# Performance work log

Measured on AMD Instinct MI355X. Metric: run time of the kernel, lower is better.

Reference implementation:

```python
import jax, jax.numpy as jnp
import numpy as np

E = 8          # num_experts
K = 2          # top_k
CAP = 0.8      # capacity_ratio
LN_EPS = 1e-6


def setup_inputs() -> dict:
    key = jax.random.key(0)
    ks = jax.random.split(key, 6)
    N, C, H, W = 64, 384, 32, 32
    Hd = 4 * C
    x = jax.random.normal(ks[0], (N, C, H, W), jnp.float32)
    conv_w = jax.random.normal(ks[1], (7, 7, 1, C), jnp.float32) * 0.05  # HWIO, depthwise
    conv_b = jnp.zeros((C,), jnp.float32)
    ln_g = jnp.ones((C,), jnp.float32)
    ln_b = jnp.zeros((C,), jnp.float32)
    gate_w = jax.random.normal(ks[2], (E, C), jnp.float32) * 0.02
    w1 = jax.random.normal(ks[3], (E, C, Hd), jnp.float32) * 0.02
    b1 = jnp.zeros((E, Hd), jnp.float32)
    w2 = jax.random.normal(ks[4], (E, Hd, C), jnp.float32) * 0.02
    b2 = jnp.zeros((E, C), jnp.float32)
    layer_scale = jnp.ones((C, 1, 1), jnp.float32) * 1e-6
    return dict(x=x, conv_w=conv_w, conv_b=conv_b, ln_g=ln_g, ln_b=ln_b,
                gate_w=gate_w, w1=w1, b1=b1, w2=w2, b2=b2, layer_scale=layer_scale)


def reference(x, conv_w, conv_b, ln_g, ln_b, gate_w, w1, b1, w2, b2, layer_scale):
    N, C, H, W = x.shape
    # depthwise 7x7 conv, pad 3
    h = jax.lax.conv_general_dilated(
        x, conv_w, window_strides=(1, 1), padding=[(3, 3), (3, 3)],
        dimension_numbers=('NCHW', 'HWIO', 'NCHW'), feature_group_count=C)
    h = h + conv_b[None, :, None, None]
    h = h.transpose(0, 2, 3, 1)  # NHWC
    # LayerNorm over channels
    mu = h.mean(-1, keepdims=True)
    var = ((h - mu) ** 2).mean(-1, keepdims=True)
    h = (h - mu) * jax.lax.rsqrt(var + LN_EPS) * ln_g + ln_b

    T = N * H * W
    x_flat = h.reshape(T, C)

    # Router (eval mode: no aux loss)
    logits = x_flat @ gate_w.T                    # [T, E]
    probs = jax.nn.softmax(logits, axis=-1)
    priority = probs.max(-1)                       # [T]
    topv, topi = jax.lax.top_k(logits, K)          # [T, K]
    weights = jax.nn.softmax(topv, axis=-1)        # [T, K]
    order = jnp.argsort(-priority)                 # descending priority

    # Dispatch: layout k-major like torch (order.repeat(K), topi[order].T.reshape(-1))
    token_idx = jnp.tile(order, K)                 # [M]
    expert_id = topi[order].T.reshape(-1)          # [M]
    gate = weights[order].T.reshape(-1)            # [M]
    M = K * T
    perm = jnp.argsort(expert_id, stable=True)
    token_idx = token_idx[perm]
    expert_id = expert_id[perm]
    gate = gate[perm]

    Be = int(round(K * T * CAP / E))               # static capacity per expert
    counts = jnp.bincount(expert_id, length=E)
    starts = jnp.cumsum(counts) - counts
    pos = jnp.arange(M) - starts[expert_id]
    keep = pos < Be
    slot = jnp.where(keep, expert_id * Be + pos, E * Be)  # dropped -> trash slot

    disp_tok = jnp.zeros((E * Be + 1,), jnp.int32).at[slot].set(token_idx.astype(jnp.int32))
    disp_gate = jnp.zeros((E * Be + 1,), x_flat.dtype).at[slot].set(gate)
    disp_tok = disp_tok[:-1].reshape(E, Be)
    disp_gate = disp_gate[:-1].reshape(E, Be)      # 0 for unfilled slots

    # Grouped expert MLP
    x_e = x_flat[disp_tok]                         # [E, Be, C]
    hid = jax.nn.gelu(jnp.einsum('ebc,ech->ebh', x_e, w1) + b1[:, None, :], approximate=False)
    y = (jnp.einsum('ebh,ehc->ebc', hid, w2) + b2[:, None, :]) * disp_gate[:, :, None]

    # Combine (scatter-add); unfilled slots contribute 0 (gate==0)
    out = jnp.zeros((T, C), x_flat.dtype).at[disp_tok.reshape(-1)].add(y.reshape(-1, C))

    out = out.reshape(N, H, W, C).transpose(0, 3, 1, 2)  # back to NCHW
    return x + layer_scale[None] * out
```

## Files before the change

kernel.cpp:

```cpp
#include <hip/hip_runtime.h>


typedef unsigned int u32;
typedef unsigned long long u64;
typedef unsigned short u16;
typedef __attribute__((ext_vector_type(8))) __bf16 bf16x8;
typedef __attribute__((ext_vector_type(4))) float f32x4;

#define T_TOK 65536
#define C_DIM 384
#define HD 1536
#define BE 13107
#define BP 13184

__device__ __forceinline__ u16 f2bf(float f) {
  u32 u = __float_as_uint(f);
  u32 r = (u + 0x7FFFu + ((u >> 16) & 1u)) >> 16;
  return (u16)r;
}
__device__ __forceinline__ float bf2f(u16 b) { return __uint_as_float(((u32)b) << 16); }

__device__ __forceinline__ u32 cvtpk(float a, float b) {
  u32 r;
  asm("v_cvt_pk_bf16_f32 %0, %1, %2" : "=v"(r) : "v"(a), "v"(b));
  return r;
}

__device__ __forceinline__ void gl16(const void* g, void* l) {
  __builtin_amdgcn_global_load_lds((const __attribute__((address_space(1))) void*)g,
                                   (__attribute__((address_space(3))) void*)l, 16, 0, 0);
}

__global__ __launch_bounds__(256) void k_conv(const float* __restrict__ x,
                                              const float* __restrict__ cw,
                                              const float* __restrict__ cb,
                                              float* __restrict__ hconv) {
  __shared__ float xp[38 * 38];
  int b = blockIdx.x;
  int c = b % 384;
  int tid = threadIdx.x;
  float w49[49];
#pragma unroll
  for (int i = 0; i < 49; i++) w49[i] = cw[i * 384 + c];
  float bias = cb[c];
  for (int i = tid; i < 38 * 38; i += 256) xp[i] = 0.0f;
  __syncthreads();
  const float* xsrc = x + (size_t)b * 1024;
  {
    float4 v = *(const float4*)&xsrc[tid * 4];
    int yy = tid >> 3, xx = (tid & 7) * 4;
    float* d = &xp[(yy + 3) * 38 + xx + 3];
    d[0] = v.x; d[1] = v.y; d[2] = v.z; d[3] = v.w;
  }
  __syncthreads();
  int cl = tid & 31, r0 = (tid >> 5) << 2;
  float o0 = bias, o1 = bias, o2 = bias, o3 = bias;
  const float* colbase = &xp[r0 * 38 + cl];
#pragma unroll
  for (int kx = 0; kx < 7; kx++) {
    float v[10];
#pragma unroll
    for (int k = 0; k < 10; k++) v[k] = colbase[k * 38 + kx];
#pragma unroll
    for (int ky = 0; ky < 7; ky++) {
      float wt = w49[ky * 7 + kx];
      o0 += wt * v[ky + 0];
      o1 += wt * v[ky + 1];
      o2 += wt * v[ky + 2];
      o3 += wt * v[ky + 3];
    }
  }
  float* dst = &hconv[(size_t)b * 1024 + r0 * 32 + cl];
  dst[0] = o0;
  dst[32] = o1;
  dst[64] = o2;
  dst[96] = o3;
}

__global__ __launch_bounds__(256) void k_ln(const float* __restrict__ hconv,
                                            const float* __restrict__ lng,
                                            const float* __restrict__ lnb,
                                            u16* __restrict__ xln) {
  __shared__ float tile[384 * 33];
  int nb = blockIdx.x;
  int n = nb >> 5, y = nb & 31;
  int tid = threadIdx.x;
  const float* src = hconv + (size_t)n * 384 * 1024 + (y << 5);
  for (int i = tid; i < 12288; i += 256) {
    int c = i >> 5, w = i & 31;
    tile[c * 33 + w] = src[(size_t)c * 1024 + w];
  }
  __syncthreads();
  int wv = tid >> 6, lane = tid & 63;
  for (int w = wv; w < 32; w += 4) {
    float v[6];
    float s = 0.f, s2 = 0.f;
#pragma unroll
    for (int k = 0; k < 6; k++) {
      float t = tile[(lane + (k << 6)) * 33 + w];
      v[k] = t; s += t; s2 += t * t;
    }
#pragma unroll
    for (int off = 32; off > 0; off >>= 1) {
      s += __shfl_xor(s, off, 64);
      s2 += __shfl_xor(s2, off, 64);
    }
    float mu = s * (1.0f / 384.0f);
    float var = s2 * (1.0f / 384.0f) - mu * mu;
    float r = rsqrtf(var + 1e-6f);
    size_t t0 = ((size_t)nb << 5) + w;
#pragma unroll
    for (int k = 0; k < 6; k++) {
      int c = lane + (k << 6);
      float o = (v[k] - mu) * r * lng[c] + lnb[c];
      xln[t0 * 384 + c] = f2bf(o);
    }
  }
}

__global__ __launch_bounds__(256) void k_router(const u16* __restrict__ xln,
                                                const float* __restrict__ gw,
                                                u32* __restrict__ keys, u32* __restrict__ vals,
                                                u32* __restrict__ topi,
                                                float* __restrict__ g1, float* __restrict__ g2) {
  __shared__ float gwl[8 * 384];
  int tid = threadIdx.x;
  for (int i = tid; i < 3072; i += 256) gwl[i] = gw[i];
  __syncthreads();
  int wv = tid >> 6, lane = tid & 63;
  int t = (blockIdx.x << 2) + wv;
  float acc[8] = {0, 0, 0, 0, 0, 0, 0, 0};
#pragma unroll
  for (int k = 0; k < 6; k++) {
    int c = lane + (k << 6);
    float xv = bf2f(xln[(size_t)t * 384 + c]);
#pragma unroll
    for (int e = 0; e < 8; e++) acc[e] += xv * gwl[e * 384 + c];
  }
#pragma unroll
  for (int off = 32; off > 0; off >>= 1) {
#pragma unroll
    for (int e = 0; e < 8; e++) acc[e] += __shfl_xor(acc[e], off, 64);
  }
  if (lane == 0) {
    float v1 = -1e30f, v2 = -1e30f;
    int e1 = 0, e2 = 0;
#pragma unroll
    for (int e = 0; e < 8; e++) {
      float l = acc[e];
      if (l > v1) { v2 = v1; e2 = e1; v1 = l; e1 = e; }
      else if (l > v2) { v2 = l; e2 = e; }
    }
    float sum = 0.f;
#pragma unroll
    for (int e = 0; e < 8; e++) sum += __expf(acc[e] - v1);
    float p = 1.0f / sum;
    float ew = __expf(v2 - v1);
    float w1 = 1.0f / (1.0f + ew);
    keys[t] = (~__float_as_uint(p)) >> 16;
    vals[t] = (u32)t;
    topi[t] = (u32)e1 | ((u32)e2 << 8);
    g1[t] = w1;
    g2[t] = ew * w1;
  }
}

__global__ __launch_bounds__(256) void k_hist(const u32* __restrict__ keys,
                                              u32* __restrict__ hist, int shift) {
  __shared__ u32 h[256];
  int tid = threadIdx.x;
  h[tid] = 0;
  __syncthreads();
  u32 key = keys[((size_t)blockIdx.x << 8) + tid];
  atomicAdd(&h[(key >> shift) & 255u], 1u);
  __syncthreads();
  hist[(size_t)tid * gridDim.x + blockIdx.x] = h[tid];
}

__global__ __launch_bounds__(256) void k_scan_rows(u32* __restrict__ data,
                                                   u32* __restrict__ totals, int nb) {
  __shared__ u32 ws[256];
  int d = blockIdx.x, tid = threadIdx.x;
  int seg = nb >> 8;
  u32 base = (u32)d * nb + tid * seg;
  u32 v[2] = {0, 0};
  u32 s = 0;
  for (int i = 0; i < seg; i++) { v[i] = data[base + i]; s += v[i]; }
  ws[tid] = s;
  __syncthreads();
  for (int dd = 1; dd < 256; dd <<= 1) {
    u32 t = (tid >= dd) ? ws[tid - dd] : 0u;
    __syncthreads();
    ws[tid] += t;
    __syncthreads();
  }
  if (tid == 255) totals[d] = ws[255];
  u32 run = (tid > 0) ? ws[tid - 1] : 0u;
  for (int i = 0; i < seg; i++) {
    u32 tmp = v[i];
    data[base + i] = run;
    run += tmp;
  }
}

__global__ __launch_bounds__(256) void k_scan_digits(const u32* __restrict__ totals,
                                                     u32* __restrict__ dbase) {
  __shared__ u32 ws[256];
  int tid = threadIdx.x;
  ws[tid] = totals[tid];
  __syncthreads();
  for (int dd = 1; dd < 256; dd <<= 1) {
    u32 t = (tid >= dd) ? ws[tid - dd] : 0u;
    __syncthreads();
    ws[tid] += t;
    __syncthreads();
  }
  dbase[tid] = (tid > 0) ? ws[tid - 1] : 0u;
}

__global__ __launch_bounds__(256) void k_scatter(const u32* __restrict__ kin,
                                                 const u32* __restrict__ vin,
                                                 u32* __restrict__ kout, u32* __restrict__ vout,
                                                 const u32* __restrict__ scanned,
                                                 const u32* __restrict__ dbase, int shift) {
  __shared__ u32 cnt[4 * 256];
  int tid = threadIdx.x;
  int w = tid >> 6, l = tid & 63;
  int g = (blockIdx.x << 8) + tid;
  u32 key = kin[g], val = vin[g];
  u32 d = (key >> shift) & 255u;
  for (int i = tid; i < 1024; i += 256) cnt[i] = 0u;
  __syncthreads();
  u64 match = ~0ull;
#pragma unroll
  for (int b = 0; b < 8; b++) {
    int bit = (d >> b) & 1;
    u64 bal = __ballot(bit);
    match &= bit ? bal : ~bal;
  }
  u32 rw = __popcll(match & ((1ull << l) - 1ull));
  if (rw == 0) cnt[(w << 8) + d] = (u32)__popcll(match);
  __syncthreads();
  u32 pre = 0;
  for (int w2 = 0; w2 < w; w2++) pre += cnt[(w2 << 8) + d];
  u32 pos = dbase[d] + scanned[(size_t)d * gridDim.x + blockIdx.x] + pre + rw;
  kout[pos] = key;
  vout[pos] = val;
}

__global__ __launch_bounds__(256) void k_entries(const u32* __restrict__ order,
                                                 const u32* __restrict__ topi,
                                                 const float* __restrict__ g1,
                                                 const float* __restrict__ g2,
                                                 u32* __restrict__ ee, u32* __restrict__ et,
                                                 float* __restrict__ eg) {
  int m = (blockIdx.x << 8) + threadIdx.x;
  int i = m & 65535, k = m >> 16;
  u32 tok = order[i];
  u32 pk = topi[tok];
  ee[m] = k ? ((pk >> 8) & 255u) : (pk & 255u);
  et[m] = tok;
  eg[m] = k ? g2[tok] : g1[tok];
}

__global__ __launch_bounds__(256) void k_dispatch(const u32* __restrict__ ee,
                                                  const u32* __restrict__ et,
                                                  const float* __restrict__ eg,
                                                  const u32* __restrict__ scanned,
                                                  int* __restrict__ dtok, float* __restrict__ dgate,
                                                  int* __restrict__ inv) {
  __shared__ u32 cnt[4 * 8];
  int tid = threadIdx.x;
  int w = tid >> 6, l = tid & 63;
  int m = (blockIdx.x << 8) + tid;
  u32 e = ee[m];
  if (tid < 32) cnt[tid] = 0u;
  __syncthreads();
  u64 match = ~0ull;
#pragma unroll
  for (int b = 0; b < 3; b++) {
    int bit = (e >> b) & 1;
    u64 bal = __ballot(bit);
    match &= bit ? bal : ~bal;
  }
  u32 rw = __popcll(match & ((1ull << l) - 1ull));
  if (rw == 0) cnt[(w << 3) + e] = (u32)__popcll(match);
  __syncthreads();
  u32 pre = 0;
  for (int w2 = 0; w2 < w; w2++) pre += cnt[(w2 << 3) + e];
  u32 pos = scanned[(size_t)e * gridDim.x + blockIdx.x] + pre + rw;
  if (pos < (u32)BE) {
    int slot = (int)e * BP + (int)pos;
    dtok[slot] = (int)et[m];
    dgate[slot] = eg[m];
    inv[et[m] * 2 + (m >> 16)] = slot;
  }
}

__global__ __launch_bounds__(256) void k_pack(const float* __restrict__ w,
                                              u16* __restrict__ wp, int NKK, int S) {
  __shared__ float tile[32 * 132];
  int e = blockIdx.y;
  int bx = blockIdx.x;
  int by = bx / NKK, kk = bx - by * NKK;
  int tid = threadIdx.x;
  const float* src = w + ((size_t)e * NKK * 32 + (size_t)kk * 32) * S + by * 128;
  for (int i = tid; i < 4096; i += 256) {
    int r = i >> 7, c = i & 127;
    tile[r * 132 + c] = src[(size_t)r * S + c];
  }
  __syncthreads();
  u16* dst = wp + ((size_t)e * gridDim.x + bx) * 4096;
#pragma unroll
  for (int h = 0; h < 2; h++) {
    int f = tid + (h << 8);
    int lane6 = f & 63, grp = f >> 6;
    int m15 = lane6 & 15, kq = lane6 >> 4;
    u16 o[8];
#pragma unroll
    for (int j = 0; j < 8; j++) o[j] = f2bf(tile[(kq * 8 + j) * 132 + grp * 16 + m15]);
    *(uint4*)&dst[f * 8] = *(const uint4*)o;
  }
}

__global__ __launch_bounds__(256) void k_gather(const u16* __restrict__ xln,
                                                const int* __restrict__ dtok,
                                                u16* __restrict__ apack, int e0) {
  __shared__ int stok[128];
  int b = blockIdx.x;
  int zloc = b / 103, bx = b - zloc * 103;
  int e = e0 + zloc;
  int tid = threadIdx.x;
  if (tid < 128) stok[tid] = dtok[e * BP + bx * 128 + tid];
  __syncthreads();
  u16* dst = apack + (size_t)b * 12 * 4096;
  int f0 = tid, f1 = tid + 256;
  int g0 = f0 >> 6, l0 = f0 & 63;
  int g1 = f1 >> 6, l1 = f1 & 63;
  int tokA = stok[g0 * 16 + (l0 & 15)];
  int tokB = stok[g1 * 16 + (l1 & 15)];
  const u16* sA = xln + (size_t)tokA * 384 + (l0 >> 4) * 8;
  const u16* sB = xln + (size_t)tokB * 384 + (l1 >> 4) * 8;
  u16* dA = dst + f0 * 8;
  u16* dB = dst + f1 * 8;
#pragma unroll
  for (int kk = 0; kk < 12; kk++) {
    *(uint4*)(dA + kk * 4096) = *(const uint4*)(sA + kk * 32);
    *(uint4*)(dB + kk * 4096) = *(const uint4*)(sB + kk * 32);
  }
}

__global__ __launch_bounds__(256) void k_gemm1(const u16* __restrict__ apack,
                                               const u16* __restrict__ w1p,
                                               const float* __restrict__ b1,
                                               u16* __restrict__ hid, int e0) {
  __shared__ __align__(16) char smem[49152];
  int tid = threadIdx.x;
  int bid = blockIdx.x;
  int lg = (bid & 7) * 618 + (bid >> 3);
  int z = lg / 1236;
  int rr = lg - z * 1236;
  int bx = rr / 12;
  int by = rr - bx * 12;
  int e = e0 + z;
  int wv = tid >> 6, lane = tid & 63;
  int wm = wv & 1, wn = wv >> 1;
  int quad = lane >> 4, c15 = lane & 15;
  const u16* asrc = apack + ((size_t)(z * 103 + bx) * 12) * 4096;
  const u16* bsrc = w1p + ((size_t)(e * 12 + by) * 12) * 4096;
  float4 bias4[4];
#pragma unroll
  for (int j = 0; j < 4; j++)
    bias4[j] = *(const float4*)&b1[e * HD + by * 128 + wn * 64 + j * 16 + quad * 4];
  f32x4 acc[4][4];
#pragma unroll
  for (int i = 0; i < 4; i++)
#pragma unroll
    for (int j = 0; j < 4; j++) acc[i][j] = (f32x4){0.f, 0.f, 0.f, 0.f};

  char* const bb0 = smem;
  char* const bb1 = smem + 16384;
  char* const bb2 = smem + 32768;

  auto issue = [&](int kk, char* buf) {
    short* As = (short*)buf;
    short* Bs = (short*)(buf + 8192);
    const u16* a = asrc + kk * 4096;
    const u16* b = bsrc + kk * 4096;
    gl16(a + tid * 8, &As[tid * 8]);
    gl16(a + (tid + 256) * 8, &As[(tid + 256) * 8]);
    gl16(b + tid * 8, &Bs[tid * 8]);
    gl16(b + (tid + 256) * 8, &Bs[(tid + 256) * 8]);
  };
  auto compute = [&](char* buf) {
    short* As = (short*)buf;
    short* Bs = (short*)(buf + 8192);
    bf16x8 af[4], bfr[4];
#pragma unroll
    for (int i = 0; i < 4; i++) af[i] = *(const bf16x8*)&As[((((wm << 2) + i) << 6) | lane) * 8];
#pragma unroll
    for (int j = 0; j < 4; j++) bfr[j] = *(const bf16x8*)&Bs[((((wn << 2) + j) << 6) | lane) * 8];
    __builtin_amdgcn_s_setprio(1);
#pragma unroll
    for (int i = 0; i < 4; i++)
#pragma unroll
      for (int j = 0; j < 4; j++)
        acc[i][j] = __builtin_amdgcn_mfma_f32_16x16x32_bf16(bfr[j], af[i], acc[i][j], 0, 0, 0);
    __builtin_amdgcn_s_setprio(0);
  };

  asm volatile("s_waitcnt vmcnt(0) lgkmcnt(0)" ::: "memory");
  __builtin_amdgcn_sched_barrier(0);
  issue(0, bb0);
  issue(1, bb1);
#define STEP1(tt, ib, cb)                                \
  issue(tt + 2, ib);                                     \
  asm volatile("s_waitcnt vmcnt(8)" ::: "memory");       \
  __builtin_amdgcn_sched_barrier(0);                     \
  __builtin_amdgcn_s_barrier();                          \
  compute(cb);                                           \
  __builtin_amdgcn_s_barrier();
  for (int t0 = 0; t0 < 9; t0 += 3) {
    STEP1(t0, bb2, bb0)
    STEP1(t0 + 1, bb0, bb1)
    STEP1(t0 + 2, bb1, bb2)
  }
  STEP1(9, bb2, bb0)
#undef STEP1
  asm volatile("s_waitcnt vmcnt(4)" ::: "memory");
  __builtin_amdgcn_sched_barrier(0);
  __builtin_amdgcn_s_barrier();
  compute(bb1);
  asm volatile("s_waitcnt vmcnt(0)" ::: "memory");
  __builtin_amdgcn_sched_barrier(0);
  __builtin_amdgcn_s_barrier();
  compute(bb2);
  __syncthreads();

  u16* prp = (u16*)smem + wv * 4608;
#pragma unroll
  for (int j = 0; j < 4; j++) {
    float4 b4 = bias4[j];
    int ncol = j * 16 + quad * 4;
#pragma unroll
    for (int i = 0; i < 4; i++) {
      int mrow = i * 16 + c15;
      float v0 = acc[i][j][0] + b4.x;
      float v1 = acc[i][j][1] + b4.y;
      float v2 = acc[i][j][2] + b4.z;
      float v3 = acc[i][j][3] + b4.w;
      v0 *= __builtin_amdgcn_rcpf(1.0f + __expf(-1.702f * v0));
      v1 *= __builtin_amdgcn_rcpf(1.0f + __expf(-1.702f * v1));
      v2 *= __builtin_amdgcn_rcpf(1.0f + __expf(-1.702f * v2));
      v3 *= __builtin_amdgcn_rcpf(1.0f + __expf(-1.702f * v3));
      uint2 pk;
      pk.x = cvtpk(v0, v1);
      pk.y = cvtpk(v2, v3);
      *(uint2*)&prp[mrow * 72 + ncol] = pk;
    }
  }
  u16* hb = hid + ((size_t)(z * 103 + bx) * 48 + by * 4 + wn * 2) * 4096 + (wm * 4) * 512 + lane * 8;
#pragma unroll
  for (int k2 = 0; k2 < 2; k2++)
#pragma unroll
    for (int gs = 0; gs < 4; gs++) {
      uint4 v = *(const uint4*)&prp[(gs * 16 + c15) * 72 + k2 * 32 + quad * 8];
      *(uint4*)(hb + (size_t)k2 * 4096 + gs * 512) = v;
    }
}

__global__ __launch_bounds__(256) void k_gemm2(const u16* __restrict__ hid,
                                               const u16* __restrict__ w2p,
                                               const float* __restrict__ b2,
                                               const float* __restrict__ dgate,
                                               u16* __restrict__ yb, int e0) {
  __shared__ __align__(16) char smem[49152];
  int tid = threadIdx.x;
  int bid = blockIdx.x;
  int xcd = bid & 7;
  int lg = xcd * 154 + (xcd < 4 ? xcd : 4) + (bid >> 3);
  int z = lg / 309;
  int rr = lg - z * 309;
  int bx = rr / 3;
  int byn = rr - bx * 3;
  int e = e0 + z;
  int wv = tid >> 6, lane = tid & 63;
  int wm = wv & 1, wn = wv >> 1;
  int quad = lane >> 4, c15 = lane & 15;
  const u16* asrc = hid + ((size_t)(z * 103 + bx) * 48) * 4096;
  const u16* bsrc = w2p + ((size_t)(e * 3 + byn) * 48) * 4096;
  float4 bias4[4];
#pragma unroll
  for (int j = 0; j < 4; j++)
    bias4[j] = *(const float4*)&b2[e * 384 + byn * 128 + wn * 64 + j * 16 + quad * 4];
  float gv[4];
#pragma unroll
  for (int i = 0; i < 4; i++) gv[i] = dgate[e * BP + bx * 128 + wm * 64 + i * 16 + c15];
  f32x4 acc[4][4];
#pragma unroll
  for (int i = 0; i < 4; i++)
#pragma unroll
    for (int j = 0; j < 4; j++) acc[i][j] = (f32x4){0.f, 0.f, 0.f, 0.f};

  char* const bb0 = smem;
  char* const bb1 = smem + 16384;
  char* const bb2 = smem + 32768;

  auto issue = [&](int kk, char* buf) {
    short* As = (short*)buf;
    short* Bs = (short*)(buf + 8192);
    const u16* a = asrc + kk * 4096;
    const u16* b = bsrc + kk * 4096;
    gl16(a + tid * 8, &As[tid * 8]);
    gl16(a + (tid + 256) * 8, &As[(tid + 256) * 8]);
    gl16(b + tid * 8, &Bs[tid * 8]);
    gl16(b + (tid + 256) * 8, &Bs[(tid + 256) * 8]);
  };
  auto compute = [&](char* buf) {
    short* As = (short*)buf;
    short* Bs = (short*)(buf + 8192);
    bf16x8 af[4], bfr[4];
#pragma unroll
    for (int i = 0; i < 4; i++) af[i] = *(const bf16x8*)&As[((((wm << 2) + i) << 6) | lane) * 8];
#pragma unroll
    for (int j = 0; j < 4; j++) bfr[j] = *(const bf16x8*)&Bs[((((wn << 2) + j) << 6) | lane) * 8];
    __builtin_amdgcn_s_setprio(1);
#pragma unroll
    for (int i = 0; i < 4; i++)
#pragma unroll
      for (int j = 0; j < 4; j++)
        acc[i][j] = __builtin_amdgcn_mfma_f32_16x16x32_bf16(bfr[j], af[i], acc[i][j], 0, 0, 0);
    __builtin_amdgcn_s_setprio(0);
  };

  asm volatile("s_waitcnt vmcnt(0) lgkmcnt(0)" ::: "memory");
  __builtin_amdgcn_sched_barrier(0);
  issue(0, bb0);
  issue(1, bb1);
#define STEP2(tt, ib, cb)                                \
  issue(tt + 2, ib);                                     \
  asm volatile("s_waitcnt vmcnt(8)" ::: "memory");       \
  __builtin_amdgcn_sched_barrier(0);                     \
  __builtin_amdgcn_s_barrier();                          \
  compute(cb);                                           \
  __builtin_amdgcn_s_barrier();
  for (int t0 = 0; t0 < 45; t0 += 3) {
    STEP2(t0, bb2, bb0)
    STEP2(t0 + 1, bb0, bb1)
    STEP2(t0 + 2, bb1, bb2)
  }
  STEP2(45, bb2, bb0)
#undef STEP2
  asm volatile("s_waitcnt vmcnt(4)" ::: "memory");
  __builtin_amdgcn_sched_barrier(0);
  __builtin_amdgcn_s_barrier();
  compute(bb1);
  asm volatile("s_waitcnt vmcnt(0)" ::: "memory");
  __builtin_amdgcn_sched_barrier(0);
  __builtin_amdgcn_s_barrier();
  compute(bb2);
  __syncthreads();

  u16* prp = (u16*)smem + wv * 4608;
#pragma unroll
  for (int j = 0; j < 4; j++) {
    float4 b4 = bias4[j];
    int ncol = j * 16 + quad * 4;
#pragma unroll
    for (int i = 0; i < 4; i++) {
      int mrow = i * 16 + c15;
      float g = gv[i];
      float v0 = (acc[i][j][0] + b4.x) * g;
      float v1 = (acc[i][j][1] + b4.y) * g;
      float v2 = (acc[i][j][2] + b4.z) * g;
      float v3 = (acc[i][j][3] + b4.w) * g;
      uint2 pk;
      pk.x = cvtpk(v0, v1);
      pk.y = cvtpk(v2, v3);
      *(uint2*)&prp[mrow * 72 + ncol] = pk;
    }
  }
  u16* ybase = yb + ((size_t)(e * BP + bx * 128 + wm * 64)) * 384 + byn * 128 + wn * 64;
#pragma unroll
  for (int it = 0; it < 8; it++) {
    int r = it * 8 + (lane >> 3);
    int n0 = (lane & 7) * 8;
    uint4 v = *(const uint4*)&prp[r * 72 + n0];
    *(uint4*)(ybase + (size_t)r * 384 + n0) = v;
  }
}

__global__ __launch_bounds__(256) void k_final(const float* __restrict__ x,
                                               const u16* __restrict__ yb,
                                               const int* __restrict__ inv,
                                               const float* __restrict__ ls,
                                               float* __restrict__ out) {
  __shared__ float tile[32 * 385];
  __shared__ int sl[64];
  int nb = blockIdx.x;
  int n = nb >> 5, yy = nb & 31;
  int tid = threadIdx.x;
  int t0 = nb << 5;
  if (tid < 64) sl[tid] = inv[t0 * 2 + tid];
  __syncthreads();
  for (int idx = tid; idx < 1536; idx += 256) {
    int w = idx / 48;
    int cc = (idx - w * 48) << 3;
    float a[8] = {0, 0, 0, 0, 0, 0, 0, 0};
#pragma unroll
    for (int k = 0; k < 2; k++) {
      int s = sl[(w << 1) + k];
      if (s >= 0) {
        uint4 v = *(const uint4*)&yb[(size_t)s * 384 + cc];
        const u16* pv = (const u16*)&v;
#pragma unroll
        for (int j = 0; j < 8; j++) a[j] += bf2f(pv[j]);
      }
    }
    float* tp = &tile[w * 385 + cc];
#pragma unroll
    for (int j = 0; j < 8; j++) tp[j] = a[j];
  }
  __syncthreads();
  for (int i2 = tid; i2 < 3072; i2 += 256) {
    int c = i2 >> 3, w4 = (i2 & 7) << 2;
    size_t o = ((((size_t)n * 384 + c) << 5) + yy) * 32 + w4;
    float4 xv = *(const float4*)&x[o];
    float lsv = ls[c];
    float4 r;
    r.x = xv.x + lsv * tile[(w4 + 0) * 385 + c];
    r.y = xv.y + lsv * tile[(w4 + 1) * 385 + c];
    r.z = xv.z + lsv * tile[(w4 + 2) * 385 + c];
    r.w = xv.w + lsv * tile[(w4 + 3) * 385 + c];
    *(float4*)&out[o] = r;
  }
}

extern "C" void kernel_launch(void* const* d_in, const int* in_sizes, int n_in,
                              void* d_out, int out_size, void* d_ws, size_t ws_size,
                              hipStream_t stream) {
  (void)in_sizes; (void)n_in; (void)out_size; (void)ws_size;
  const float* x     = (const float*)d_in[0];
  const float* convw = (const float*)d_in[1];
  const float* convb = (const float*)d_in[2];
  const float* lng   = (const float*)d_in[3];
  const float* lnb   = (const float*)d_in[4];
  const float* gw    = (const float*)d_in[5];
  const float* w1    = (const float*)d_in[6];
  const float* b1    = (const float*)d_in[7];
  const float* w2    = (const float*)d_in[8];
  const float* b2    = (const float*)d_in[9];
  const float* ls    = (const float*)d_in[10];
  float* out = (float*)d_out;

  char* p = (char*)d_ws;
  size_t o = 0;
  auto alloc = [&](size_t b) { void* r = p + o; o += (b + 255) & ~(size_t)255; return r; };
  u16* xln    = (u16*)alloc((size_t)T_TOK * C_DIM * 2);
  u16* w1p    = (u16*)alloc((size_t)8 * 144 * 4096 * 2);
  u16* w2p    = (u16*)alloc((size_t)8 * 144 * 4096 * 2);
  u16* hid    = (u16*)alloc((size_t)4 * BP * HD * 2);
  u16* yb     = (u16*)alloc((size_t)8 * BP * 384 * 2);
  u16* apack  = (u16*)alloc((size_t)4 * 103 * 12 * 4096 * 2);
  u32* keysA  = (u32*)alloc((size_t)T_TOK * 4);
  u32* keysB  = (u32*)alloc((size_t)T_TOK * 4);
  u32* valsA  = (u32*)alloc((size_t)T_TOK * 4);
  u32* valsB  = (u32*)alloc((size_t)T_TOK * 4);
  u32* topi   = (u32*)alloc((size_t)T_TOK * 4);
  float* g1   = (float*)alloc((size_t)T_TOK * 4);
  float* g2   = (float*)alloc((size_t)T_TOK * 4);
  u32* hist   = (u32*)alloc((size_t)256 * 512 * 4);
  u32* totals = (u32*)alloc((size_t)256 * 4);
  u32* dbase  = (u32*)alloc((size_t)256 * 4);
  u32* ee     = (u32*)alloc((size_t)131072 * 4);
  u32* et     = (u32*)alloc((size_t)131072 * 4);
  float* eg   = (float*)alloc((size_t)131072 * 4);
  int* dtok   = (int*)alloc((size_t)8 * BP * 4);
  float* dgate= (float*)alloc((size_t)8 * BP * 4);
  int* inv    = (int*)alloc((size_t)T_TOK * 2 * 4);

  float* hconv = (float*)hid;

  k_conv<<<24576, 256, 0, stream>>>(x, convw, convb, hconv);
  k_ln<<<2048, 256, 0, stream>>>(hconv, lng, lnb, xln);
  k_router<<<16384, 256, 0, stream>>>(xln, gw, keysA, valsA, topi, g1, g2);

  u32 *ki = keysA, *vi = valsA, *ko = keysB, *vo = valsB;
  for (int pass = 0; pass < 2; pass++) {
    int shift = pass * 8;
    k_hist<<<256, 256, 0, stream>>>(ki, hist, shift);
    k_scan_rows<<<256, 256, 0, stream>>>(hist, totals, 256);
    k_scan_digits<<<1, 256, 0, stream>>>(totals, dbase);
    k_scatter<<<256, 256, 0, stream>>>(ki, vi, ko, vo, hist, dbase, shift);
    u32* t1 = ki; ki = ko; ko = t1;
    u32* t2 = vi; vi = vo; vo = t2;
  }
  k_entries<<<512, 256, 0, stream>>>(vi, topi, g1, g2, ee, et, eg);
  k_hist<<<512, 256, 0, stream>>>(ee, hist, 0);
  k_scan_rows<<<256, 256, 0, stream>>>(hist, totals, 512);
  hipMemsetAsync(dtok, 0, (size_t)8 * BP * 4, stream);
  hipMemsetAsync(dgate, 0, (size_t)8 * BP * 4, stream);
  hipMemsetAsync(inv, 0xFF, (size_t)T_TOK * 2 * 4, stream);
  k_dispatch<<<512, 256, 0, stream>>>(ee, et, eg, hist, dtok, dgate, inv);

  k_pack<<<dim3(144, 8), 256, 0, stream>>>(w1, w1p, 12, 1536);
  k_pack<<<dim3(144, 8), 256, 0, stream>>>(w2, w2p, 48, 384);

  for (int g = 0; g < 2; g++) {
    k_gather<<<412, 256, 0, stream>>>(xln, dtok, apack, g * 4);
    k_gemm1<<<4944, 256, 0, stream>>>(apack, w1p, b1, hid, g * 4);
    k_gemm2<<<1236, 256, 0, stream>>>(hid, w2p, b2, dgate, yb, g * 4);
  }
  k_final<<<2048, 256, 0, stream>>>(x, yb, inv, ls, out);
}
```

Before: 712.2 us.

## Store conv output as bf16 and switch expert GEMMs to double buffering

The depthwise conv now writes its intermediate as bf16 instead of fp32, which halves the bytes written by the conv and read by the LayerNorm kernel. Both grouped expert GEMM kernels drop from a 3-stage to a 2-stage LDS pipeline, cutting shared memory from 48KB to 36KB per block so more blocks can fit per CU. The trade-offs are extra rounding of the conv output before LayerNorm, and a shallower prefetch depth, since each load now has only one compute step to hide its latency.

```diff
diff --git a/kernel.cpp b/kernel.cpp
--- a/kernel.cpp
+++ b/kernel.cpp
@@ -34,7 +34,7 @@
 __global__ __launch_bounds__(256) void k_conv(const float* __restrict__ x,
                                               const float* __restrict__ cw,
                                               const float* __restrict__ cb,
-                                              float* __restrict__ hconv) {
+                                              u16* __restrict__ hconv) {
   __shared__ float xp[38 * 38];
   int b = blockIdx.x;
   int c = b % 384;
@@ -70,14 +70,14 @@
       o3 += wt * v[ky + 3];
     }
   }
-  float* dst = &hconv[(size_t)b * 1024 + r0 * 32 + cl];
-  dst[0] = o0;
-  dst[32] = o1;
-  dst[64] = o2;
-  dst[96] = o3;
-}
-
-__global__ __launch_bounds__(256) void k_ln(const float* __restrict__ hconv,
+  u16* dst = &hconv[(size_t)b * 1024 + r0 * 32 + cl];
+  dst[0]  = f2bf(o0);
+  dst[32] = f2bf(o1);
+  dst[64] = f2bf(o2);
+  dst[96] = f2bf(o3);
+}
+
+__global__ __launch_bounds__(256) void k_ln(const u16* __restrict__ hconv,
                                             const float* __restrict__ lng,
                                             const float* __restrict__ lnb,
                                             u16* __restrict__ xln) {
@@ -85,10 +85,10 @@
   int nb = blockIdx.x;
   int n = nb >> 5, y = nb & 31;
   int tid = threadIdx.x;
-  const float* src = hconv + (size_t)n * 384 * 1024 + (y << 5);
+  const u16* src = hconv + (size_t)n * 384 * 1024 + (y << 5);
   for (int i = tid; i < 12288; i += 256) {
     int c = i >> 5, w = i & 31;
-    tile[c * 33 + w] = src[(size_t)c * 1024 + w];
+    tile[c * 33 + w] = bf2f(src[(size_t)c * 1024 + w]);
   }
   __syncthreads();
   int wv = tid >> 6, lane = tid & 63;
@@ -354,7 +354,7 @@
                                                const u16* __restrict__ w1p,
                                                const float* __restrict__ b1,
                                                u16* __restrict__ hid, int e0) {
-  __shared__ __align__(16) char smem[49152];
+  __shared__ __align__(16) char smem[36864];
   int tid = threadIdx.x;
   int bid = blockIdx.x;
   int lg = (bid & 7) * 618 + (bid >> 3);
@@ -380,7 +380,6 @@
 
   char* const bb0 = smem;
   char* const bb1 = smem + 16384;
-  char* const bb2 = smem + 32768;
 
   auto issue = [&](int kk, char* buf) {
     short* As = (short*)buf;
@@ -412,29 +411,31 @@
   asm volatile("s_waitcnt vmcnt(0) lgkmcnt(0)" ::: "memory");
   __builtin_amdgcn_sched_barrier(0);
   issue(0, bb0);
-  issue(1, bb1);
-#define STEP1(tt, ib, cb)                                \
-  issue(tt + 2, ib);                                     \
-  asm volatile("s_waitcnt vmcnt(8)" ::: "memory");       \
+#define STEPA(tt)                                        \
+  issue(tt + 1, bb1);                                    \
+  asm volatile("s_waitcnt vmcnt(4)" ::: "memory");       \
   __builtin_amdgcn_sched_barrier(0);                     \
   __builtin_amdgcn_s_barrier();                          \
-  compute(cb);                                           \
+  compute(bb0);                                          \
   __builtin_amdgcn_s_barrier();
-  for (int t0 = 0; t0 < 9; t0 += 3) {
-    STEP1(t0, bb2, bb0)
-    STEP1(t0 + 1, bb0, bb1)
-    STEP1(t0 + 2, bb1, bb2)
-  }
-  STEP1(9, bb2, bb0)
-#undef STEP1
-  asm volatile("s_waitcnt vmcnt(4)" ::: "memory");
+#define STEPB(tt)                                        \
+  issue(tt + 1, bb0);                                    \
+  asm volatile("s_waitcnt vmcnt(4)" ::: "memory");       \
+  __builtin_amdgcn_sched_barrier(0);                     \
+  __builtin_amdgcn_s_barrier();                          \
+  compute(bb1);                                          \
+  __builtin_amdgcn_s_barrier();
+  for (int t0 = 0; t0 < 10; t0 += 2) {
+    STEPA(t0)
+    STEPB(t0 + 1)
+  }
+  STEPA(10)
+#undef STEPA
+#undef STEPB
+  asm volatile("s_waitcnt vmcnt(0)" ::: "memory");
   __builtin_amdgcn_sched_barrier(0);
   __builtin_amdgcn_s_barrier();
   compute(bb1);
-  asm volatile("s_waitcnt vmcnt(0)" ::: "memory");
-  __builtin_amdgcn_sched_barrier(0);
-  __builtin_amdgcn_s_barrier();
-  compute(bb2);
   __syncthreads();
 
   u16* prp = (u16*)smem + wv * 4608;
@@ -474,7 +475,7 @@
                                                const float* __restrict__ b2,
                                                const float* __restrict__ dgate,
                                                u16* __restrict__ yb, int e0) {
-  __shared__ __align__(16) char smem[49152];
+  __shared__ __align__(16) char smem[36864];
   int tid = threadIdx.x;
   int bid = blockIdx.x;
   int xcd = bid & 7;
@@ -504,7 +505,6 @@
 
   char* const bb0 = smem;
   char* const bb1 = smem + 16384;
-  char* const bb2 = smem + 32768;
 
   auto issue = [&](int kk, char* buf) {
     short* As = (short*)buf;
@@ -536,29 +536,31 @@
   asm volatile("s_waitcnt vmcnt(0) lgkmcnt(0)" ::: "memory");
   __builtin_amdgcn_sched_barrier(0);
   issue(0, bb0);
-  issue(1, bb1);
-#define STEP2(tt, ib, cb)                                \
-  issue(tt + 2, ib);                                     \
-  asm volatile("s_waitcnt vmcnt(8)" ::: "memory");       \
+#define STEPA(tt)                                        \
+  issue(tt + 1, bb1);                                    \
+  asm volatile("s_waitcnt vmcnt(4)" ::: "memory");       \
   __builtin_amdgcn_sched_barrier(0);                     \
   __builtin_amdgcn_s_barrier();                          \
-  compute(cb);                                           \
+  compute(bb0);                                          \
   __builtin_amdgcn_s_barrier();
-  for (int t0 = 0; t0 < 45; t0 += 3) {
-    STEP2(t0, bb2, bb0)
-    STEP2(t0 + 1, bb0, bb1)
-    STEP2(t0 + 2, bb1, bb2)
-  }
-  STEP2(45, bb2, bb0)
-#undef STEP2
-  asm volatile("s_waitcnt vmcnt(4)" ::: "memory");
+#define STEPB(tt)                                        \
+  issue(tt + 1, bb0);                                    \
+  asm volatile("s_waitcnt vmcnt(4)" ::: "memory");       \
+  __builtin_amdgcn_sched_barrier(0);                     \
+  __builtin_amdgcn_s_barrier();                          \
+  compute(bb1);                                          \
+  __builtin_amdgcn_s_barrier();
+  for (int t0 = 0; t0 < 46; t0 += 2) {
+    STEPA(t0)
+    STEPB(t0 + 1)
+  }
+  STEPA(46)
+#undef STEPA
+#undef STEPB
+  asm volatile("s_waitcnt vmcnt(0)" ::: "memory");
   __builtin_amdgcn_sched_barrier(0);
   __builtin_amdgcn_s_barrier();
   compute(bb1);
-  asm volatile("s_waitcnt vmcnt(0)" ::: "memory");
-  __builtin_amdgcn_sched_barrier(0);
-  __builtin_amdgcn_s_barrier();
-  compute(bb2);
   __syncthreads();
 
   u16* prp = (u16*)smem + wv * 4608;
@@ -679,7 +681,7 @@
   float* dgate= (float*)alloc((size_t)8 * BP * 4);
   int* inv    = (int*)alloc((size_t)T_TOK * 2 * 4);
 
-  float* hconv = (float*)hid;
+  u16* hconv = (u16*)hid;
 
   k_conv<<<24576, 256, 0, stream>>>(x, convw, convb, hconv);
   k_ln<<<2048, 256, 0, stream>>>(hconv, lng, lnb, xln);
```

Measured after the change: 765.2 us. 1.07x slower.
